# Performance work log

Measured on AMD Instinct MI355X. Metric: run time of the kernel, lower is better.

The kernel has to match this reference:

```python
import jax, jax.numpy as jnp
import numpy as np

TEMP = 5.0  # temperature_init
# All C(4,2)=6 keep-2-of-4 patterns for 2:4 semi-structured sparsity
PATTERNS = jnp.array([[1,1,0,0],[1,0,1,0],[1,0,0,1],[0,1,1,0],[0,1,0,1],[0,0,1,1]], dtype=jnp.float32)


def masked_linear(x, w, b, alpha, ids):
    # x: [N, I], w: [O, I], alpha: [A, O, I//4, 6], ids: [N]
    A, O, G, P = alpha.shape
    probs = jax.nn.softmax(alpha / TEMP, axis=-1)            # [A, O, G, 6]
    mask = jnp.einsum('aogp,pk->aogk', probs, PATTERNS)      # [A, O, G, 4]
    wm = w[None, :, :] * mask.reshape(A, O, G * 4)           # [A, O, I] per-agent masked weight
    y = jnp.einsum('ni,aoi->nao', x, wm)                     # dense per-agent GEMM
    y = jnp.take_along_axis(y, ids[:, None, None], axis=1)[:, 0, :]
    return y + b


def gru_cell(x, h, w_ih, w_hh, b_ih, b_hh):
    gi = x @ w_ih.T + b_ih
    gh = h @ w_hh.T + b_hh
    i_r, i_z, i_n = jnp.split(gi, 3, axis=-1)
    h_r, h_z, h_n = jnp.split(gh, 3, axis=-1)
    r = jax.nn.sigmoid(i_r + h_r)
    z = jax.nn.sigmoid(i_z + h_z)
    n = jnp.tanh(i_n + r * h_n)
    return (1.0 - z) * n + z * h


def setup_inputs() -> dict:
    key = jax.random.key(0)
    ks = jax.random.split(key, 20)
    B, A, E, H, NA = 1024, 8, 64, 512, 16
    s = 0.05
    d = {}
    d['inputs'] = jax.random.normal(ks[0], (B, A, E), jnp.float32)
    d['hidden_state'] = jax.random.normal(ks[1], (B, A, H), jnp.float32)
    d['agent_ids'] = jax.random.randint(ks[2], (B, A), 0, A, jnp.int32)
    d['fc1_w'] = jax.random.normal(ks[3], (H, E), jnp.float32) * s
    d['fc1_b'] = jax.random.normal(ks[4], (H,), jnp.float32) * s
    d['fc1_alpha'] = jax.random.normal(ks[5], (A, H, E // 4, 6), jnp.float32)
    d['gru_w_ih'] = jax.random.normal(ks[6], (3 * H, H), jnp.float32) * s
    d['gru_w_hh'] = jax.random.normal(ks[7], (3 * H, H), jnp.float32) * s
    d['gru_b_ih'] = jax.random.normal(ks[8], (3 * H,), jnp.float32) * s
    d['gru_b_hh'] = jax.random.normal(ks[9], (3 * H,), jnp.float32) * s
    d['fc2_w'] = jax.random.normal(ks[10], (H, H), jnp.float32) * s
    d['fc2_b'] = jax.random.normal(ks[11], (H,), jnp.float32) * s
    d['fc2_alpha'] = jax.random.normal(ks[12], (A, H, H // 4, 6), jnp.float32)
    d['fc3_w'] = jax.random.normal(ks[13], (H, H), jnp.float32) * s
    d['fc3_b'] = jax.random.normal(ks[14], (H,), jnp.float32) * s
    d['fc3_alpha'] = jax.random.normal(ks[15], (A, H, H // 4, 6), jnp.float32)
    d['fc4_w'] = jax.random.normal(ks[16], (NA, H), jnp.float32) * s
    d['fc4_b'] = jax.random.normal(ks[17], (NA,), jnp.float32) * s
    d['fc4_alpha'] = jax.random.normal(ks[18], (A, NA, H // 4, 6), jnp.float32)
    return d


def reference(inputs, hidden_state, agent_ids,
              fc1_w, fc1_b, fc1_alpha,
              gru_w_ih, gru_w_hh, gru_b_ih, gru_b_hh,
              fc2_w, fc2_b, fc2_alpha,
              fc3_w, fc3_b, fc3_alpha,
              fc4_w, fc4_b, fc4_alpha):
    b, a, e = inputs.shape
    H = hidden_state.shape[-1]
    x = inputs.reshape(-1, e)
    ids = agent_ids.reshape(-1)
    x = jax.nn.relu(masked_linear(x, fc1_w, fc1_b, fc1_alpha, ids))
    h = gru_cell(x, hidden_state.reshape(-1, H), gru_w_ih, gru_w_hh, gru_b_ih, gru_b_hh)
    q = jax.nn.relu(masked_linear(h, fc2_w, fc2_b, fc2_alpha, ids))
    q = jax.nn.relu(masked_linear(q, fc3_w, fc3_b, fc3_alpha, ids))
    q = masked_linear(q, fc4_w, fc4_b, fc4_alpha, ids)
    return q.reshape(b, a, -1), h.reshape(b, a, -1)
```

## Files before the change

### kernel.cpp

```cpp
#include <hip/hip_runtime.h>
#include <hip/hip_bf16.h>

typedef unsigned short ushort_t;
typedef __bf16 bf16x8 __attribute__((ext_vector_type(8)));
typedef unsigned short us8 __attribute__((ext_vector_type(8)));
typedef float f32x4 __attribute__((ext_vector_type(4)));

__device__ __forceinline__ float b2f(ushort_t h) {
    union { unsigned int u; float f; } v; v.u = ((unsigned int)h) << 16; return v.f;
}
__device__ __forceinline__ ushort_t f2b(float f) {
    union { float f; unsigned int u; } v; v.f = f;
    unsigned int u = v.u;
    unsigned int r = (u + 0x7FFFu + ((u >> 16) & 1u)) >> 16;
    return (ushort_t)r;
}
__device__ __forceinline__ float sigmoidf_(float x) {
    return 1.f / (1.f + __expf(-x));
}
__device__ __forceinline__ void store_o(ushort_t* p, float v) { *p = f2b(v); }
__device__ __forceinline__ void store_o(float* p, float v) { *p = v; }

__global__ void fill_kernel(float* out, long long n, float val) {
    long long i = (long long)blockIdx.x * blockDim.x + threadIdx.x;
    if (i < n) out[i] = val;
}

#define PACKSZ(O, K) ((long long)((O) >= 64 ? (O) >> 6 : 1) * ((K) >> 5) * 2048)

__global__ void sort_kernel(const int* __restrict__ ids, int N,
                            int* __restrict__ perm, int* __restrict__ seg,
                            int4* __restrict__ ttab, int* __restrict__ tcount) {
    __shared__ int hist[16][8];
    __shared__ int wbase[16][8];
    __shared__ int atot[8];
    __shared__ int abase[8];
    int tid = threadIdx.x, wave = tid >> 6, lane = tid & 63;
    int base = wave * 512;
    unsigned long long lt = (lane == 63) ? 0x7fffffffffffffffull
                                         : ((1ull << lane) - 1ull);
    int myid[8], rank[8];
    int run[8] = {0, 0, 0, 0, 0, 0, 0, 0};
    #pragma unroll
    for (int i = 0; i < 8; i++) myid[i] = ids[base + i * 64 + lane] & 7;
    #pragma unroll
    for (int i = 0; i < 8; i++) {
        int a = myid[i];
        int r = 0;
        #pragma unroll
        for (int a2 = 0; a2 < 8; a2++) {
            unsigned long long m = __ballot(a == a2);
            if (a2 == a) r = run[a2] + __popcll(m & lt);
            run[a2] += __popcll(m);
        }
        rank[i] = r;
    }
    if (lane == 0) {
        #pragma unroll
        for (int a = 0; a < 8; a++) hist[wave][a] = run[a];
    }
    __syncthreads();
    if (tid < 8) {
        int a = tid, s = 0;
        for (int w = 0; w < 16; w++) { wbase[w][a] = s; s += hist[w][a]; }
        atot[a] = s;
    }
    __syncthreads();
    if (tid == 0) {
        int s = 0;
        for (int a = 0; a < 8; a++) { abase[a] = s; seg[a] = s; s += atot[a]; }
        seg[8] = s;
        int T = 0;
        for (int a = 0; a < 8; a++)
            for (int m = abase[a]; m < abase[a] + atot[a]; m += 64) {
                int e = abase[a] + atot[a];
                if (e > m + 64) e = m + 64;
                ttab[T++] = make_int4(a, m, e, 0);
            }
        *tcount = T;
    }
    __syncthreads();
    #pragma unroll
    for (int i = 0; i < 8; i++) {
        int a = myid[i];
        perm[abase[a] + wbase[wave][a] + rank[i]] = base + i * 64 + lane;
    }
}

__device__ __forceinline__ void maskw_item(const float* __restrict__ alpha,
                                           const float* __restrict__ w,
                                           ushort_t* __restrict__ wm,
                                           long long idx, int O, int G, int dup) {
    int g = (int)(idx % G);
    long long t2 = idx / G;
    int o = (int)(t2 % O);
    int a = (int)(t2 / O);
    const float* al = alpha + idx * 6;
    float p[6];
    float mx = -1e30f;
    #pragma unroll
    for (int i = 0; i < 6; i++) { p[i] = al[i] * 0.2f; mx = fmaxf(mx, p[i]); }
    float s = 0.f;
    #pragma unroll
    for (int i = 0; i < 6; i++) { p[i] = __expf(p[i] - mx); s += p[i]; }
    float inv = 1.f / s;
    #pragma unroll
    for (int i = 0; i < 6; i++) p[i] *= inv;
    float mk[4] = { p[0] + p[1] + p[2], p[0] + p[3] + p[4],
                    p[1] + p[3] + p[5], p[2] + p[4] + p[5] };
    int K = G * 4;
    const float* wr = w + (long long)o * K + g * 4;
    ushort_t* base = wm + (long long)a * PACKSZ(O, K);
    int k0 = g * 4;
    int c = o >> 6, su = (o >> 4) & 3, n = o & 15;
    int kk = k0 >> 5, q = (k0 >> 3) & 3, e0 = k0 & 7;
    long long off = (((long long)(c * (K >> 5) + kk) * 4 + su) * 64 + (q * 16 + n)) * 8 + e0;
    #pragma unroll
    for (int t = 0; t < 4; t++) {
        ushort_t v = f2b(wr[t] * mk[t]);
        base[off + t] = v;
        if (dup) {
            base[off + t + 512] = v;
            base[off + t + 1024] = v;
            base[off + t + 1536] = v;
        }
    }
}

__device__ __forceinline__ void canon_gather_item(const float* __restrict__ src,
                                                  ushort_t* __restrict__ dst,
                                                  const int* __restrict__ perm,
                                                  int ld, long long i) {
    long long base = i * 8;
    int pos = (int)(base / ld);
    int k = (int)(base % ld);
    int row = perm[pos] & 8191;
    const float* s = src + (long long)row * ld + k;
    us8 v;
    #pragma unroll
    for (int e = 0; e < 8; e++) v[e] = f2b(s[e]);
    *(us8*)(dst + base) = v;
}

__device__ __forceinline__ void canon_pack_item(const float* __restrict__ src,
                                                ushort_t* __restrict__ dst,
                                                long long i) {
    long long base = i * 8;
    int o_full = (int)(base >> 9);
    int k0 = (int)(base & 511);
    int g = o_full >> 9, o = o_full & 511;
    int c = o >> 6, su = (o >> 4) & 3, n = o & 15;
    int kk = k0 >> 5, q = (k0 >> 3) & 3;
    long long off = (long long)g * 262144 +
        (((long long)(c * 16 + kk) * 4 + su) * 64 + (q * 16 + n)) * 8;
    us8 v;
    #pragma unroll
    for (int e = 0; e < 8; e++) v[e] = f2b(src[base + e]);
    *(us8*)(dst + off) = v;
}

#define PB0 256
#define PB1 2048
#define PB2 2048
#define PB3 64
#define PB4 256
#define PB5 2048
#define PB6 384
#define PB7 384
#define PREP_BLOCKS (PB0+PB1+PB2+PB3+PB4+PB5+PB6+PB7)

__global__ void prep_kernel(const float* fc1_al, const float* fc1_w, ushort_t* wm1,
                            const float* fc2_al, const float* fc2_w, ushort_t* wm2,
                            const float* fc3_al, const float* fc3_w, ushort_t* wm3,
                            const float* fc4_al, const float* fc4_w, ushort_t* wm4,
                            const float* inputs, ushort_t* inp_pos,
                            const float* hidden, ushort_t* hid_pos,
                            const float* wih, ushort_t* wihp,
                            const float* whh, ushort_t* whhp,
                            const int* perm) {
    int b = blockIdx.x;
    int tid = threadIdx.x;
    if (b < PB0) { maskw_item(fc1_al, fc1_w, wm1, (long long)b * 256 + tid, 512, 16, 0); return; }
    b -= PB0;
    if (b < PB1) { maskw_item(fc2_al, fc2_w, wm2, (long long)b * 256 + tid, 512, 128, 0); return; }
    b -= PB1;
    if (b < PB2) { maskw_item(fc3_al, fc3_w, wm3, (long long)b * 256 + tid, 512, 128, 0); return; }
    b -= PB2;
    if (b < PB3) { maskw_item(fc4_al, fc4_w, wm4, (long long)b * 256 + tid, 16, 128, 1); return; }
    b -= PB3;
    if (b < PB4) { canon_gather_item(inputs, inp_pos, perm, 64, (long long)b * 256 + tid); return; }
    b -= PB4;
    if (b < PB5) { canon_gather_item(hidden, hid_pos, perm, 512, (long long)b * 256 + tid); return; }
    b -= PB5;
    if (b < PB6) { canon_pack_item(wih, wihp, (long long)b * 256 + tid); return; }
    b -= PB6;
    canon_pack_item(whh, whhp, (long long)b * 256 + tid);
}

#define BM 64
#define BN 64

template <typename OT>
__launch_bounds__(256, 4)
__global__ void gemm_tiled(const ushort_t* __restrict__ In, int ldin,
                           const ushort_t* __restrict__ Wpk, long long wstride,
                           const float* __restrict__ bias,
                           OT* __restrict__ Out, int ldo,
                           const int4* __restrict__ ttab,
                           const int* __restrict__ tcount,
                           const int* __restrict__ scatter,
                           int O, int K, int relu) {
    int t = blockIdx.x;
    if (t >= *tcount) return;
    int4 tt = ttab[t];
    int a = tt.x, pos0 = tt.y, pos1 = tt.z;
    int o0 = blockIdx.y * BN;

    __shared__ ushort_t As[2048];

    int tid = threadIdx.x;
    int wave = tid >> 6, lane = tid & 63;
    int wr = (wave >> 1) & 1, wc = wave & 1;
    int quad = lane >> 4, l16 = lane & 15;
    int srow = tid >> 2, sgrp = tid & 3;
    int wsoff = (srow * 4 + (sgrp ^ ((srow >> 2) & 3))) * 8;
    int rl = (l16 * 4 + (quad ^ ((l16 >> 2) & 3))) * 8;

    int apos = pos0 + srow;
    int apos_c = apos < pos1 ? apos : (pos1 - 1);
    const ushort_t* aptr = In + (long long)apos_c * ldin + sgrp * 8;

    const ushort_t* wb = Wpk + (long long)a * wstride +
        (long long)blockIdx.y * (K >> 5) * 2048 + lane * 8;

    f32x4 acc[2][2];
    #pragma unroll
    for (int i = 0; i < 2; i++)
        #pragma unroll
        for (int j = 0; j < 2; j++) acc[i][j] = (f32x4){0.f, 0.f, 0.f, 0.f};

    int KK = K >> 5;
    for (int kk = 0; kk < KK; kk++) {
        us8 av = *(const us8*)(aptr + kk * 32);
        bf16x8 bfr[2];
        bfr[0] = *(const bf16x8*)(wb + (kk * 4 + wc * 2 + 0) * 512);
        bfr[1] = *(const bf16x8*)(wb + (kk * 4 + wc * 2 + 1) * 512);
        __syncthreads();
        *(us8*)(&As[wsoff]) = av;
        __syncthreads();
        bf16x8 af[2];
        af[0] = *(const bf16x8*)(&As[(wr * 2 + 0) * 512 + rl]);
        af[1] = *(const bf16x8*)(&As[(wr * 2 + 1) * 512 + rl]);
        #pragma unroll
        for (int i = 0; i < 2; i++)
            #pragma unroll
            for (int j = 0; j < 2; j++)
                acc[i][j] = __builtin_amdgcn_mfma_f32_16x16x32_bf16(af[i], bfr[j], acc[i][j], 0, 0, 0);
    }

    #pragma unroll
    for (int i = 0; i < 2; i++) {
        int mbase = wr * 32 + i * 16 + quad * 4;
        #pragma unroll
        for (int j = 0; j < 2; j++) {
            int col = o0 + wc * 32 + j * 16 + l16;
            if (col < O) {
                float bias_v = bias ? bias[col] : 0.f;
                #pragma unroll
                for (int r = 0; r < 4; r++) {
                    int pos = pos0 + mbase + r;
                    if (pos < pos1) {
                        float v = acc[i][j][r] + bias_v;
                        if (relu) v = fmaxf(v, 0.f);
                        int orow = (scatter ? scatter[pos] : pos) & 8191;
                        store_o(&Out[(long long)orow * ldo + col], v);
                    }
                }
            }
        }
    }
}

__launch_bounds__(256, 3)
__global__ void gru_fused(const ushort_t* __restrict__ y1,
                          const ushort_t* __restrict__ hid_pos,
                          const float* __restrict__ hidden_f,
                          const ushort_t* __restrict__ wihp,
                          const ushort_t* __restrict__ whhp,
                          const float* __restrict__ bih,
                          const float* __restrict__ bhh,
                          const int* __restrict__ perm,
                          float* __restrict__ out_h_f,
                          ushort_t* __restrict__ hp,
                          int N, int H) {
    int m0 = blockIdx.x * 64;

    __shared__ ushort_t Ay[2048];
    __shared__ ushort_t Ah[2048];
    __shared__ ushort_t Bt[6][2048];

    int tid = threadIdx.x;
    int wave = tid >> 6, lane = tid & 63;
    int wr = (wave >> 1) & 1, wc = wave & 1;
    int quad = lane >> 4, l16 = lane & 15;
    int srow = tid >> 2, sgrp = tid & 3;
    int wsoff = (srow * 4 + (sgrp ^ ((srow >> 2) & 3))) * 8;
    int rl = (l16 * 4 + (quad ^ ((l16 >> 2) & 3))) * 8;

    const ushort_t* ay_p = y1 + (long long)(m0 + srow) * H + sgrp * 8;
    const ushort_t* ah_p = hid_pos + (long long)(m0 + srow) * H + sgrp * 8;

    long long cb = (long long)blockIdx.y * 16 * 2048 + tid * 8;
    const ushort_t* wbg[6];
    #pragma unroll
    for (int g = 0; g < 3; g++) wbg[g] = wihp + (long long)g * 262144 + cb;
    #pragma unroll
    for (int g = 3; g < 6; g++) wbg[g] = whhp + (long long)(g - 3) * 262144 + cb;

    f32x4 acc[4][2][2];
    #pragma unroll
    for (int g = 0; g < 4; g++)
        #pragma unroll
        for (int i = 0; i < 2; i++)
            #pragma unroll
            for (int j = 0; j < 2; j++) acc[g][i][j] = (f32x4){0.f, 0.f, 0.f, 0.f};

    for (int kk = 0; kk < 16; kk++) {
        us8 va = *(const us8*)(ay_p + kk * 32);
        us8 vh = *(const us8*)(ah_p + kk * 32);
        us8 vb[6];
        #pragma unroll
        for (int g = 0; g < 6; g++) vb[g] = *(const us8*)(wbg[g] + kk * 2048);
        __syncthreads();
        *(us8*)(&Ay[wsoff]) = va;
        *(us8*)(&Ah[wsoff]) = vh;
        #pragma unroll
        for (int g = 0; g < 6; g++) *(us8*)(&Bt[g][tid * 8]) = vb[g];
        __syncthreads();

        bf16x8 ayf[2], ahf[2];
        #pragma unroll
        for (int u = 0; u < 2; u++) {
            ayf[u] = *(const bf16x8*)(&Ay[(wr * 2 + u) * 512 + rl]);
            ahf[u] = *(const bf16x8*)(&Ah[(wr * 2 + u) * 512 + rl]);
        }
        #pragma unroll
        for (int g = 0; g < 3; g++) {
            bf16x8 bw[2], bu[2];
            #pragma unroll
            for (int u = 0; u < 2; u++) {
                bw[u] = *(const bf16x8*)(&Bt[g][(wc * 2 + u) * 512 + lane * 8]);
                bu[u] = *(const bf16x8*)(&Bt[g + 3][(wc * 2 + u) * 512 + lane * 8]);
            }
            int ai = (g < 2) ? g : 2;
            int ah2 = (g < 2) ? g : 3;
            #pragma unroll
            for (int i = 0; i < 2; i++)
                #pragma unroll
                for (int j = 0; j < 2; j++) {
                    acc[ai][i][j] = __builtin_amdgcn_mfma_f32_16x16x32_bf16(
                        ayf[i], bw[j], acc[ai][i][j], 0, 0, 0);
                    acc[ah2][i][j] = __builtin_amdgcn_mfma_f32_16x16x32_bf16(
                        ahf[i], bu[j], acc[ah2][i][j], 0, 0, 0);
                }
        }
    }

    int c0 = blockIdx.y * 64;
    #pragma unroll
    for (int i = 0; i < 2; i++) {
        #pragma unroll
        for (int r = 0; r < 4; r++) {
            int pos = m0 + wr * 32 + i * 16 + quad * 4 + r;
            int norig = perm[pos] & 8191;
            #pragma unroll
            for (int j = 0; j < 2; j++) {
                int col = c0 + wc * 32 + j * 16 + l16;
                float sr = acc[0][i][j][r] + bih[col] + bhh[col];
                float sz = acc[1][i][j][r] + bih[H + col] + bhh[H + col];
                float in_ = acc[2][i][j][r] + bih[2 * H + col];
                float hn = acc[3][i][j][r] + bhh[2 * H + col];
                float rg = sigmoidf_(sr);
                float zg = sigmoidf_(sz);
                float ng = tanhf(in_ + rg * hn);
                float hv = hidden_f[(long long)norig * H + col];
                float hnew = (1.f - zg) * ng + zg * hv;
                out_h_f[(long long)norig * H + col] = hnew;
                hp[(long long)pos * H + col] = f2b(hnew);
            }
        }
    }
}

extern "C" void kernel_launch(void* const* d_in, const int* in_sizes, int n_in,
                              void* d_out, int out_size, void* d_ws, size_t ws_size,
                              hipStream_t stream) {
    (void)in_sizes; (void)n_in;
    const int N = 8192, A = 8, E = 64, H = 512, NA = 16;

    float* out_f = (float*)d_out;
    float* out_q = out_f;
    float* out_h = out_f + (size_t)N * NA;

    char* p = (char*)d_ws;
    auto alloc = [&](size_t b) { char* r = p; p += (b + 255) & ~(size_t)255; return r; };
    int*  perm   = (int*)alloc((size_t)N * 4);
    int*  seg    = (int*)alloc(16 * 4);
    int4* ttab   = (int4*)alloc(144 * 16);
    int*  tcount = (int*)alloc(256);
    ushort_t* wm1     = (ushort_t*)alloc((size_t)A * PACKSZ(H, E) * 2);
    ushort_t* wm2     = (ushort_t*)alloc((size_t)A * PACKSZ(H, H) * 2);
    ushort_t* wm3     = (ushort_t*)alloc((size_t)A * PACKSZ(H, H) * 2);
    ushort_t* wm4     = (ushort_t*)alloc((size_t)A * PACKSZ(NA, H) * 2);
    ushort_t* y1      = (ushort_t*)alloc((size_t)N * H * 2);
    ushort_t* inp_pos = (ushort_t*)alloc((size_t)N * E * 2);
    ushort_t* hid_pos = (ushort_t*)alloc((size_t)N * H * 2);
    ushort_t* wihp    = (ushort_t*)alloc((size_t)3 * H * H * 2);
    ushort_t* whhp    = (ushort_t*)alloc((size_t)3 * H * H * 2);
    ushort_t* hp      = (ushort_t*)alloc((size_t)N * H * 2);
    size_t need = (size_t)(p - (char*)d_ws);
    ushort_t* q2 = y1;
    ushort_t* q3 = hid_pos;

    if (ws_size < need) {
        fill_kernel<<<(unsigned)((out_size + 255) / 256), 256, 0, stream>>>(
            out_f, out_size, 1000.f);
        return;
    }

    const float* inputs = (const float*)d_in[0];
    const float* hidden = (const float*)d_in[1];
    const int*   ids    = (const int*)d_in[2];
    const float* fc1_w  = (const float*)d_in[3];
    const float* fc1_b  = (const float*)d_in[4];
    const float* fc1_al = (const float*)d_in[5];
    const float* wih    = (const float*)d_in[6];
    const float* whh    = (const float*)d_in[7];
    const float* bih    = (const float*)d_in[8];
    const float* bhh    = (const float*)d_in[9];
    const float* fc2_w  = (const float*)d_in[10];
    const float* fc2_b  = (const float*)d_in[11];
    const float* fc2_al = (const float*)d_in[12];
    const float* fc3_w  = (const float*)d_in[13];
    const float* fc3_b  = (const float*)d_in[14];
    const float* fc3_al = (const float*)d_in[15];
    const float* fc4_w  = (const float*)d_in[16];
    const float* fc4_b  = (const float*)d_in[17];
    const float* fc4_al = (const float*)d_in[18];

    sort_kernel<<<1, 1024, 0, stream>>>(ids, N, perm, seg, ttab, tcount);

    prep_kernel<<<PREP_BLOCKS, 256, 0, stream>>>(
        fc1_al, fc1_w, wm1, fc2_al, fc2_w, wm2, fc3_al, fc3_w, wm3,
        fc4_al, fc4_w, wm4, inputs, inp_pos, hidden, hid_pos,
        wih, wihp, whh, whhp, perm);

    dim3 blk(256);
    gemm_tiled<ushort_t><<<dim3(136, H / BN), blk, 0, stream>>>(
        inp_pos, E, wm1, PACKSZ(H, E), fc1_b, y1, H, ttab, tcount,
        nullptr, H, E, 1);
    gru_fused<<<dim3(N / 64, H / 64), blk, 0, stream>>>(
        y1, hid_pos, hidden, wihp, whhp, bih, bhh, perm, out_h, hp, N, H);
    gemm_tiled<ushort_t><<<dim3(136, H / BN), blk, 0, stream>>>(
        hp, H, wm2, PACKSZ(H, H), fc2_b, q2, H, ttab, tcount,
        nullptr, H, H, 1);
    gemm_tiled<ushort_t><<<dim3(136, H / BN), blk, 0, stream>>>(
        q2, H, wm3, PACKSZ(H, H), fc3_b, q3, H, ttab, tcount,
        nullptr, H, H, 1);
    gemm_tiled<float><<<dim3(136, 1), blk, 0, stream>>>(
        q3, H, wm4, PACKSZ(NA, H), fc4_b, out_q, NA, ttab, tcount,
        perm, NA, H, 0);
}
```

Measured before the change: 228.3 us.

## Pre-pack activations in MFMA fragment layout with padded agent segments, drop LDS staging

```diff
diff --git a/kernel.cpp b/kernel.cpp
--- a/kernel.cpp
+++ b/kernel.cpp
@@ -6,9 +6,9 @@
 typedef unsigned short us8 __attribute__((ext_vector_type(8)));
 typedef float f32x4 __attribute__((ext_vector_type(4)));
 
-__device__ __forceinline__ float b2f(ushort_t h) {
-    union { unsigned int u; float f; } v; v.u = ((unsigned int)h) << 16; return v.f;
-}
+#define NPAD 8704
+#define SENT (1 << 20)
+
 __device__ __forceinline__ ushort_t f2b(float f) {
     union { float f; unsigned int u; } v; v.f = f;
     unsigned int u = v.u;
@@ -18,8 +18,6 @@
 __device__ __forceinline__ float sigmoidf_(float x) {
     return 1.f / (1.f + __expf(-x));
 }
-__device__ __forceinline__ void store_o(ushort_t* p, float v) { *p = f2b(v); }
-__device__ __forceinline__ void store_o(float* p, float v) { *p = v; }
 
 __global__ void fill_kernel(float* out, long long n, float val) {
     long long i = (long long)blockIdx.x * blockDim.x + threadIdx.x;
@@ -68,15 +66,20 @@
     __syncthreads();
     if (tid == 0) {
         int s = 0;
-        for (int a = 0; a < 8; a++) { abase[a] = s; seg[a] = s; s += atot[a]; }
+        for (int a = 0; a < 8; a++) {
+            abase[a] = s; seg[a] = s;
+            s += (atot[a] + 63) & ~63;
+        }
         seg[8] = s;
         int T = 0;
-        for (int a = 0; a < 8; a++)
-            for (int m = abase[a]; m < abase[a] + atot[a]; m += 64) {
-                int e = abase[a] + atot[a];
-                if (e > m + 64) e = m + 64;
-                ttab[T++] = make_int4(a, m, e, 0);
+        for (int a = 0; a < 8; a++) {
+            int e = abase[a] + atot[a];
+            int pe = abase[a] + ((atot[a] + 63) & ~63);
+            for (int m = abase[a]; m < pe; m += 64) {
+                int z = e < m + 64 ? e : m + 64;
+                ttab[T++] = make_int4(a, m, z, 0);
             }
+        }
         *tcount = T;
     }
     __syncthreads();
@@ -85,6 +88,13 @@
         int a = myid[i];
         perm[abase[a] + wbase[wave][a] + rank[i]] = base + i * 64 + lane;
     }
+    for (int a = 0; a < 8; a++) {
+        int e = abase[a] + atot[a];
+        int pe = abase[a] + ((atot[a] + 63) & ~63);
+        for (int p2 = e + tid; p2 < pe; p2 += 1024) perm[p2] = SENT;
+    }
+    int Pend = abase[7] + ((atot[7] + 63) & ~63);
+    for (int p2 = Pend + tid; p2 < NPAD; p2 += 1024) perm[p2] = SENT;
 }
 
 __device__ __forceinline__ void maskw_item(const float* __restrict__ alpha,
@@ -127,19 +137,21 @@
     }
 }
 
-__device__ __forceinline__ void canon_gather_item(const float* __restrict__ src,
-                                                  ushort_t* __restrict__ dst,
-                                                  const int* __restrict__ perm,
-                                                  int ld, long long i) {
-    long long base = i * 8;
-    int pos = (int)(base / ld);
-    int k = (int)(base % ld);
-    int row = perm[pos] & 8191;
-    const float* s = src + (long long)row * ld + k;
+__device__ __forceinline__ void canon_gather_packed(const float* __restrict__ src,
+                                                    ushort_t* __restrict__ dst,
+                                                    const int* __restrict__ perm,
+                                                    int ld, long long i) {
+    int l = (int)(i & 63);
+    int tt = (int)(i >> 6);
+    int KK = ld >> 5;
+    int mt = tt / KK, kk = tt - mt * KK;
+    int row = perm[mt * 16 + (l & 15)];
+    if (row >= 8192) row = 0;
+    const float* s = src + (long long)row * ld + kk * 32 + (l >> 4) * 8;
     us8 v;
     #pragma unroll
     for (int e = 0; e < 8; e++) v[e] = f2b(s[e]);
-    *(us8*)(dst + base) = v;
+    *(us8*)(dst + i * 8) = v;
 }
 
 __device__ __forceinline__ void canon_pack_item(const float* __restrict__ src,
@@ -163,8 +175,8 @@
 #define PB1 2048
 #define PB2 2048
 #define PB3 64
-#define PB4 256
-#define PB5 2048
+#define PB4 272
+#define PB5 2176
 #define PB6 384
 #define PB7 384
 #define PREP_BLOCKS (PB0+PB1+PB2+PB3+PB4+PB5+PB6+PB7)
@@ -188,92 +200,122 @@
     b -= PB2;
     if (b < PB3) { maskw_item(fc4_al, fc4_w, wm4, (long long)b * 256 + tid, 16, 128, 1); return; }
     b -= PB3;
-    if (b < PB4) { canon_gather_item(inputs, inp_pos, perm, 64, (long long)b * 256 + tid); return; }
+    if (b < PB4) { canon_gather_packed(inputs, inp_pos, perm, 64, (long long)b * 256 + tid); return; }
     b -= PB4;
-    if (b < PB5) { canon_gather_item(hidden, hid_pos, perm, 512, (long long)b * 256 + tid); return; }
+    if (b < PB5) { canon_gather_packed(hidden, hid_pos, perm, 512, (long long)b * 256 + tid); return; }
     b -= PB5;
     if (b < PB6) { canon_pack_item(wih, wihp, (long long)b * 256 + tid); return; }
     b -= PB6;
     canon_pack_item(whh, whhp, (long long)b * 256 + tid);
 }
 
-#define BM 64
-#define BN 64
-
-template <typename OT>
+template <typename OT, int NC, int PACKOUT>
 __launch_bounds__(256, 4)
-__global__ void gemm_tiled(const ushort_t* __restrict__ In, int ldin,
+__global__ void gemm_tiled(const ushort_t* __restrict__ Apk, int K,
                            const ushort_t* __restrict__ Wpk, long long wstride,
                            const float* __restrict__ bias,
                            OT* __restrict__ Out, int ldo,
                            const int4* __restrict__ ttab,
                            const int* __restrict__ tcount,
-                           const int* __restrict__ scatter,
-                           int O, int K, int relu) {
+                           const int* __restrict__ perm,
+                           int O, int relu) {
     int t = blockIdx.x;
     if (t >= *tcount) return;
     int4 tt = ttab[t];
-    int a = tt.x, pos0 = tt.y, pos1 = tt.z;
-    int o0 = blockIdx.y * BN;
-
-    __shared__ ushort_t As[2048];
+    int a = tt.x, pos0 = tt.y;
+    constexpr int JJ = 2 * NC;
 
     int tid = threadIdx.x;
     int wave = tid >> 6, lane = tid & 63;
     int wr = (wave >> 1) & 1, wc = wave & 1;
     int quad = lane >> 4, l16 = lane & 15;
-    int srow = tid >> 2, sgrp = tid & 3;
-    int wsoff = (srow * 4 + (sgrp ^ ((srow >> 2) & 3))) * 8;
-    int rl = (l16 * 4 + (quad ^ ((l16 >> 2) & 3))) * 8;
-
-    int apos = pos0 + srow;
-    int apos_c = apos < pos1 ? apos : (pos1 - 1);
-    const ushort_t* aptr = In + (long long)apos_c * ldin + sgrp * 8;
-
+
+    int KK = K >> 5;
+    int KKh = KK >> 1;
+    int c_idx = blockIdx.y * NC + (NC == 2 ? wc : 0);
     const ushort_t* wb = Wpk + (long long)a * wstride +
-        (long long)blockIdx.y * (K >> 5) * 2048 + lane * 8;
-
-    f32x4 acc[2][2];
+        (long long)c_idx * KK * 2048 + lane * 8;
+    const ushort_t* ap = Apk + (long long)(pos0 >> 4) * KK * 512 + lane * 8;
+
+    f32x4 acc[2][JJ];
     #pragma unroll
     for (int i = 0; i < 2; i++)
         #pragma unroll
-        for (int j = 0; j < 2; j++) acc[i][j] = (f32x4){0.f, 0.f, 0.f, 0.f};
-
-    int KK = K >> 5;
-    for (int kk = 0; kk < KK; kk++) {
-        us8 av = *(const us8*)(aptr + kk * 32);
-        bf16x8 bfr[2];
-        bfr[0] = *(const bf16x8*)(wb + (kk * 4 + wc * 2 + 0) * 512);
-        bfr[1] = *(const bf16x8*)(wb + (kk * 4 + wc * 2 + 1) * 512);
-        __syncthreads();
-        *(us8*)(&As[wsoff]) = av;
-        __syncthreads();
-        bf16x8 af[2];
-        af[0] = *(const bf16x8*)(&As[(wr * 2 + 0) * 512 + rl]);
-        af[1] = *(const bf16x8*)(&As[(wr * 2 + 1) * 512 + rl]);
+        for (int j = 0; j < JJ; j++) acc[i][j] = (f32x4){0.f, 0.f, 0.f, 0.f};
+
+    bf16x8 aA[2], bA[JJ], aB[2], bB[JJ];
+
+#define GLOADS(AR, BR, kkv) do {                                              \
+    _Pragma("unroll") for (int i2 = 0; i2 < 2; i2++)                          \
+        AR[i2] = *(const bf16x8*)(ap + ((long long)(wr * 2 + i2) * KK + (kkv)) * 512); \
+    _Pragma("unroll") for (int j2 = 0; j2 < JJ; j2++) {                       \
+        int su = (NC == 2) ? j2 : wc * 2 + j2;                                \
+        BR[j2] = *(const bf16x8*)(wb + ((kkv) * 4 + su) * 512); }             \
+} while (0)
+#define GMFMAS(AR, BR) do {                                                   \
+    _Pragma("unroll") for (int i2 = 0; i2 < 2; i2++)                          \
+        _Pragma("unroll") for (int j2 = 0; j2 < JJ; j2++)                     \
+            acc[i2][j2] = __builtin_amdgcn_mfma_f32_16x16x32_bf16(            \
+                AR[i2], BR[j2], acc[i2][j2], 0, 0, 0);                        \
+} while (0)
+
+    GLOADS(aA, bA, 0);
+    #pragma unroll 1
+    for (int kk2 = 0; kk2 < KKh; kk2++) {
+        GLOADS(aB, bB, kk2 * 2 + 1);
+        GMFMAS(aA, bA);
+        if (kk2 + 1 < KKh) GLOADS(aA, bA, kk2 * 2 + 2);
+        GMFMAS(aB, bB);
+    }
+#undef GLOADS
+#undef GMFMAS
+
+    if constexpr (PACKOUT) {
+        __shared__ ushort_t Cs[64 * 136];
         #pragma unroll
         for (int i = 0; i < 2; i++)
             #pragma unroll
-            for (int j = 0; j < 2; j++)
-                acc[i][j] = __builtin_amdgcn_mfma_f32_16x16x32_bf16(af[i], bfr[j], acc[i][j], 0, 0, 0);
-    }
-
-    #pragma unroll
-    for (int i = 0; i < 2; i++) {
-        int mbase = wr * 32 + i * 16 + quad * 4;
-        #pragma unroll
-        for (int j = 0; j < 2; j++) {
-            int col = o0 + wc * 32 + j * 16 + l16;
-            if (col < O) {
-                float bias_v = bias ? bias[col] : 0.f;
+            for (int j = 0; j < JJ; j++) {
+                int colL = (NC == 2 ? wc * 64 : wc * 32) + j * 16 + l16;
+                int col = blockIdx.y * (64 * NC) + colL;
+                float bv = bias[col];
                 #pragma unroll
                 for (int r = 0; r < 4; r++) {
-                    int pos = pos0 + mbase + r;
-                    if (pos < pos1) {
-                        float v = acc[i][j][r] + bias_v;
-                        if (relu) v = fmaxf(v, 0.f);
-                        int orow = (scatter ? scatter[pos] : pos) & 8191;
-                        store_o(&Out[(long long)orow * ldo + col], v);
+                    float v = acc[i][j][r] + bv;
+                    if (relu) v = fmaxf(v, 0.f);
+                    Cs[(wr * 32 + i * 16 + quad * 4 + r) * 136 + colL] = f2b(v);
+                }
+            }
+        __syncthreads();
+        int KKo = ldo >> 5;
+        int kk0 = blockIdx.y * (2 * NC);
+        constexpr int NKK = 2 * NC;
+        #pragma unroll
+        for (int s2 = 0; s2 < NKK; s2++) {
+            int slot = s2 * 256 + tid;
+            int l = slot & 63, t4 = slot >> 6;
+            int mt = t4 / NKK, kkL = t4 - mt * NKK;
+            us8 v = *(const us8*)(&Cs[(mt * 16 + (l & 15)) * 136 + kkL * 32 + (l >> 4) * 8]);
+            *(us8*)((ushort_t*)Out + ((long long)((pos0 >> 4) + mt) * KKo + kk0 + kkL) * 512 + l * 8) = v;
+        }
+    } else {
+        #pragma unroll
+        for (int i = 0; i < 2; i++) {
+            int mbase = wr * 32 + i * 16 + quad * 4;
+            #pragma unroll
+            for (int j = 0; j < JJ; j++) {
+                int col = (NC == 2 ? wc * 64 : wc * 32) + j * 16 + l16;
+                if (col < O) {
+                    float bv = bias[col];
+                    #pragma unroll
+                    for (int r = 0; r < 4; r++) {
+                        int pos = pos0 + mbase + r;
+                        int orow = perm[pos];
+                        if (orow < 8192) {
+                            float v = acc[i][j][r] + bv;
+                            if (relu) v = fmaxf(v, 0.f);
+                            Out[(long long)orow * ldo + col] = v;
+                        }
                     }
                 }
             }
@@ -281,9 +323,9 @@
     }
 }
 
-__launch_bounds__(256, 3)
+__launch_bounds__(256, 2)
 __global__ void gru_fused(const ushort_t* __restrict__ y1,
-                          const ushort_t* __restrict__ hid_pos,
+                          const ushort_t* __restrict__ hid,
                           const float* __restrict__ hidden_f,
                           const ushort_t* __restrict__ wihp,
                           const ushort_t* __restrict__ whhp,
@@ -292,25 +334,23 @@
                           const int* __restrict__ perm,
                           float* __restrict__ out_h_f,
                           ushort_t* __restrict__ hp,
-                          int N, int H) {
-    int m0 = blockIdx.x * 64;
-
-    __shared__ ushort_t Ay[2048];
-    __shared__ ushort_t Ah[2048];
-    __shared__ ushort_t Bt[6][2048];
+                          const int4* __restrict__ ttab,
+                          const int* __restrict__ tcount,
+                          int H) {
+    int t = blockIdx.x;
+    if (t >= *tcount) return;
+    int pos0 = ttab[t].y;
+    int mt0 = pos0 >> 4;
 
     int tid = threadIdx.x;
     int wave = tid >> 6, lane = tid & 63;
     int wr = (wave >> 1) & 1, wc = wave & 1;
     int quad = lane >> 4, l16 = lane & 15;
-    int srow = tid >> 2, sgrp = tid & 3;
-    int wsoff = (srow * 4 + (sgrp ^ ((srow >> 2) & 3))) * 8;
-    int rl = (l16 * 4 + (quad ^ ((l16 >> 2) & 3))) * 8;
-
-    const ushort_t* ay_p = y1 + (long long)(m0 + srow) * H + sgrp * 8;
-    const ushort_t* ah_p = hid_pos + (long long)(m0 + srow) * H + sgrp * 8;
-
-    long long cb = (long long)blockIdx.y * 16 * 2048 + tid * 8;
+
+    const ushort_t* ayp = y1 + (long long)mt0 * 16 * 512 + lane * 8;
+    const ushort_t* ahp = hid + (long long)mt0 * 16 * 512 + lane * 8;
+
+    long long cb = (long long)blockIdx.y * 16 * 2048 + lane * 8;
     const ushort_t* wbg[6];
     #pragma unroll
     for (int g = 0; g < 3; g++) wbg[g] = wihp + (long long)g * 262144 + cb;
@@ -325,57 +365,55 @@
             #pragma unroll
             for (int j = 0; j < 2; j++) acc[g][i][j] = (f32x4){0.f, 0.f, 0.f, 0.f};
 
-    for (int kk = 0; kk < 16; kk++) {
-        us8 va = *(const us8*)(ay_p + kk * 32);
-        us8 vh = *(const us8*)(ah_p + kk * 32);
-        us8 vb[6];
-        #pragma unroll
-        for (int g = 0; g < 6; g++) vb[g] = *(const us8*)(wbg[g] + kk * 2048);
-        __syncthreads();
-        *(us8*)(&Ay[wsoff]) = va;
-        *(us8*)(&Ah[wsoff]) = vh;
-        #pragma unroll
-        for (int g = 0; g < 6; g++) *(us8*)(&Bt[g][tid * 8]) = vb[g];
-        __syncthreads();
-
-        bf16x8 ayf[2], ahf[2];
-        #pragma unroll
-        for (int u = 0; u < 2; u++) {
-            ayf[u] = *(const bf16x8*)(&Ay[(wr * 2 + u) * 512 + rl]);
-            ahf[u] = *(const bf16x8*)(&Ah[(wr * 2 + u) * 512 + rl]);
-        }
-        #pragma unroll
-        for (int g = 0; g < 3; g++) {
-            bf16x8 bw[2], bu[2];
-            #pragma unroll
-            for (int u = 0; u < 2; u++) {
-                bw[u] = *(const bf16x8*)(&Bt[g][(wc * 2 + u) * 512 + lane * 8]);
-                bu[u] = *(const bf16x8*)(&Bt[g + 3][(wc * 2 + u) * 512 + lane * 8]);
-            }
-            int ai = (g < 2) ? g : 2;
-            int ah2 = (g < 2) ? g : 3;
-            #pragma unroll
-            for (int i = 0; i < 2; i++)
-                #pragma unroll
-                for (int j = 0; j < 2; j++) {
-                    acc[ai][i][j] = __builtin_amdgcn_mfma_f32_16x16x32_bf16(
-                        ayf[i], bw[j], acc[ai][i][j], 0, 0, 0);
-                    acc[ah2][i][j] = __builtin_amdgcn_mfma_f32_16x16x32_bf16(
-                        ahf[i], bu[j], acc[ah2][i][j], 0, 0, 0);
-                }
-        }
-    }
-
+    bf16x8 ayA[2], ahA[2], bbA[6][2];
+    bf16x8 ayB[2], ahB[2], bbB[6][2];
+
+#define RLOADS(AY, AH, BB, kkv) do {                                          \
+    _Pragma("unroll") for (int i2 = 0; i2 < 2; i2++) {                        \
+        AY[i2] = *(const bf16x8*)(ayp + ((long long)(wr * 2 + i2) * 16 + (kkv)) * 512); \
+        AH[i2] = *(const bf16x8*)(ahp + ((long long)(wr * 2 + i2) * 16 + (kkv)) * 512); } \
+    _Pragma("unroll") for (int g2 = 0; g2 < 6; g2++)                          \
+        _Pragma("unroll") for (int u2 = 0; u2 < 2; u2++)                      \
+            BB[g2][u2] = *(const bf16x8*)(wbg[g2] + ((kkv) * 4 + wc * 2 + u2) * 512); \
+} while (0)
+#define RMFMAS(AY, AH, BB) do {                                               \
+    _Pragma("unroll") for (int g2 = 0; g2 < 3; g2++) {                        \
+        int ai = (g2 < 2) ? g2 : 2;                                           \
+        int ah2 = (g2 < 2) ? g2 : 3;                                          \
+        _Pragma("unroll") for (int i2 = 0; i2 < 2; i2++)                      \
+            _Pragma("unroll") for (int j2 = 0; j2 < 2; j2++) {                \
+                acc[ai][i2][j2] = __builtin_amdgcn_mfma_f32_16x16x32_bf16(    \
+                    AY[i2], BB[g2][j2], acc[ai][i2][j2], 0, 0, 0);            \
+                acc[ah2][i2][j2] = __builtin_amdgcn_mfma_f32_16x16x32_bf16(   \
+                    AH[i2], BB[g2 + 3][j2], acc[ah2][i2][j2], 0, 0, 0); } }   \
+} while (0)
+
+    RLOADS(ayA, ahA, bbA, 0);
+    #pragma unroll 1
+    for (int kk2 = 0; kk2 < 8; kk2++) {
+        RLOADS(ayB, ahB, bbB, kk2 * 2 + 1);
+        RMFMAS(ayA, ahA, bbA);
+        if (kk2 < 7) RLOADS(ayA, ahA, bbA, kk2 * 2 + 2);
+        RMFMAS(ayB, ahB, bbB);
+    }
+#undef RLOADS
+#undef RMFMAS
+
+    __shared__ ushort_t Cs[64 * 72];
     int c0 = blockIdx.y * 64;
     #pragma unroll
     for (int i = 0; i < 2; i++) {
         #pragma unroll
         for (int r = 0; r < 4; r++) {
-            int pos = m0 + wr * 32 + i * 16 + quad * 4 + r;
-            int norig = perm[pos] & 8191;
+            int rowL = wr * 32 + i * 16 + quad * 4 + r;
+            int pos = pos0 + rowL;
+            int norig = perm[pos];
+            bool realr = norig < 8192;
+            int nr = realr ? norig : 0;
             #pragma unroll
             for (int j = 0; j < 2; j++) {
-                int col = c0 + wc * 32 + j * 16 + l16;
+                int colL = wc * 32 + j * 16 + l16;
+                int col = c0 + colL;
                 float sr = acc[0][i][j][r] + bih[col] + bhh[col];
                 float sz = acc[1][i][j][r] + bih[H + col] + bhh[H + col];
                 float in_ = acc[2][i][j][r] + bih[2 * H + col];
@@ -383,12 +421,21 @@
                 float rg = sigmoidf_(sr);
                 float zg = sigmoidf_(sz);
                 float ng = tanhf(in_ + rg * hn);
-                float hv = hidden_f[(long long)norig * H + col];
+                float hv = hidden_f[(long long)nr * H + col];
                 float hnew = (1.f - zg) * ng + zg * hv;
-                out_h_f[(long long)norig * H + col] = hnew;
-                hp[(long long)pos * H + col] = f2b(hnew);
+                if (realr) out_h_f[(long long)norig * H + col] = hnew;
+                Cs[rowL * 72 + colL] = f2b(hnew);
             }
         }
+    }
+    __syncthreads();
+    #pragma unroll
+    for (int s2 = 0; s2 < 2; s2++) {
+        int slot = s2 * 256 + tid;
+        int l = slot & 63, t4 = slot >> 6;
+        int mt = t4 >> 1, kkL = t4 & 1;
+        us8 v = *(const us8*)(&Cs[(mt * 16 + (l & 15)) * 72 + kkL * 32 + (l >> 4) * 8]);
+        *(us8*)(hp + ((long long)(mt0 + mt) * 16 + blockIdx.y * 2 + kkL) * 512 + l * 8) = v;
     }
 }
 
@@ -404,7 +451,7 @@
 
     char* p = (char*)d_ws;
     auto alloc = [&](size_t b) { char* r = p; p += (b + 255) & ~(size_t)255; return r; };
-    int*  perm   = (int*)alloc((size_t)N * 4);
+    int*  perm   = (int*)alloc((size_t)NPAD * 4);
     int*  seg    = (int*)alloc(16 * 4);
     int4* ttab   = (int4*)alloc(144 * 16);
     int*  tcount = (int*)alloc(256);
@@ -412,12 +459,12 @@
     ushort_t* wm2     = (ushort_t*)alloc((size_t)A * PACKSZ(H, H) * 2);
     ushort_t* wm3     = (ushort_t*)alloc((size_t)A * PACKSZ(H, H) * 2);
     ushort_t* wm4     = (ushort_t*)alloc((size_t)A * PACKSZ(NA, H) * 2);
-    ushort_t* y1      = (ushort_t*)alloc((size_t)N * H * 2);
-    ushort_t* inp_pos = (ushort_t*)alloc((size_t)N * E * 2);
-    ushort_t* hid_pos = (ushort_t*)alloc((size_t)N * H * 2);
+    ushort_t* y1      = (ushort_t*)alloc((size_t)NPAD * H * 2);
+    ushort_t* inp_pos = (ushort_t*)alloc((size_t)NPAD * E * 2);
+    ushort_t* hid_pos = (ushort_t*)alloc((size_t)NPAD * H * 2);
     ushort_t* wihp    = (ushort_t*)alloc((size_t)3 * H * H * 2);
     ushort_t* whhp    = (ushort_t*)alloc((size_t)3 * H * H * 2);
-    ushort_t* hp      = (ushort_t*)alloc((size_t)N * H * 2);
+    ushort_t* hp      = (ushort_t*)alloc((size_t)NPAD * H * 2);
     size_t need = (size_t)(p - (char*)d_ws);
     ushort_t* q2 = y1;
     ushort_t* q3 = hid_pos;
@@ -456,18 +503,19 @@
         wih, wihp, whh, whhp, perm);
 
     dim3 blk(256);
-    gemm_tiled<ushort_t><<<dim3(136, H / BN), blk, 0, stream>>>(
+    gemm_tiled<ushort_t, 2, 1><<<dim3(136, H / 128), blk, 0, stream>>>(
         inp_pos, E, wm1, PACKSZ(H, E), fc1_b, y1, H, ttab, tcount,
-        nullptr, H, E, 1);
-    gru_fused<<<dim3(N / 64, H / 64), blk, 0, stream>>>(
-        y1, hid_pos, hidden, wihp, whhp, bih, bhh, perm, out_h, hp, N, H);
-    gemm_tiled<ushort_t><<<dim3(136, H / BN), blk, 0, stream>>>(
+        perm, H, 1);
+    gru_fused<<<dim3(136, H / 64), blk, 0, stream>>>(
+        y1, hid_pos, hidden, wihp, whhp, bih, bhh, perm, out_h, hp,
+        ttab, tcount, H);
+    gemm_tiled<ushort_t, 2, 1><<<dim3(136, H / 128), blk, 0, stream>>>(
         hp, H, wm2, PACKSZ(H, H), fc2_b, q2, H, ttab, tcount,
-        nullptr, H, H, 1);
-    gemm_tiled<ushort_t><<<dim3(136, H / BN), blk, 0, stream>>>(
+        perm, H, 1);
+    gemm_tiled<ushort_t, 2, 1><<<dim3(136, H / 128), blk, 0, stream>>>(
         q2, H, wm3, PACKSZ(H, H), fc3_b, q3, H, ttab, tcount,
-        nullptr, H, H, 1);
-    gemm_tiled<float><<<dim3(136, 1), blk, 0, stream>>>(
+        perm, H, 1);
+    gemm_tiled<float, 1, 0><<<dim3(136, 1), blk, 0, stream>>>(
         q3, H, wm4, PACKSZ(NA, H), fc4_b, out_q, NA, ttab, tcount,
-        perm, NA, H, 0);
-}
+        perm, NA, 0);
+}
```

New measurement: 246.4 us. +7.9%, slower.

## Process two K-steps per barrier in gemm_tiled and widen GRU tile to 128 rows

Applied to the files above, without the earlier changes.

```diff
diff --git a/kernel.cpp b/kernel.cpp
--- a/kernel.cpp
+++ b/kernel.cpp
@@ -6,9 +6,6 @@
 typedef unsigned short us8 __attribute__((ext_vector_type(8)));
 typedef float f32x4 __attribute__((ext_vector_type(4)));
 
-__device__ __forceinline__ float b2f(ushort_t h) {
-    union { unsigned int u; float f; } v; v.u = ((unsigned int)h) << 16; return v.f;
-}
 __device__ __forceinline__ ushort_t f2b(float f) {
     union { float f; unsigned int u; } v; v.f = f;
     unsigned int u = v.u;
@@ -216,7 +213,7 @@
     int a = tt.x, pos0 = tt.y, pos1 = tt.z;
     int o0 = blockIdx.y * BN;
 
-    __shared__ ushort_t As[2048];
+    __shared__ ushort_t As[2][2048];
 
     int tid = threadIdx.x;
     int wave = tid >> 6, lane = tid & 63;
@@ -239,23 +236,34 @@
         #pragma unroll
         for (int j = 0; j < 2; j++) acc[i][j] = (f32x4){0.f, 0.f, 0.f, 0.f};
 
-    int KK = K >> 5;
-    for (int kk = 0; kk < KK; kk++) {
-        us8 av = *(const us8*)(aptr + kk * 32);
-        bf16x8 bfr[2];
-        bfr[0] = *(const bf16x8*)(wb + (kk * 4 + wc * 2 + 0) * 512);
-        bfr[1] = *(const bf16x8*)(wb + (kk * 4 + wc * 2 + 1) * 512);
+    int KKh = K >> 6;
+    for (int k2 = 0; k2 < KKh; k2++) {
+        int kk = k2 * 2;
+        us8 av0 = *(const us8*)(aptr + kk * 32);
+        us8 av1 = *(const us8*)(aptr + kk * 32 + 32);
+        bf16x8 b00 = *(const bf16x8*)(wb + (kk * 4 + wc * 2 + 0) * 512);
+        bf16x8 b01 = *(const bf16x8*)(wb + (kk * 4 + wc * 2 + 1) * 512);
+        bf16x8 b10 = *(const bf16x8*)(wb + ((kk + 1) * 4 + wc * 2 + 0) * 512);
+        bf16x8 b11 = *(const bf16x8*)(wb + ((kk + 1) * 4 + wc * 2 + 1) * 512);
         __syncthreads();
-        *(us8*)(&As[wsoff]) = av;
+        *(us8*)(&As[0][wsoff]) = av0;
+        *(us8*)(&As[1][wsoff]) = av1;
         __syncthreads();
-        bf16x8 af[2];
-        af[0] = *(const bf16x8*)(&As[(wr * 2 + 0) * 512 + rl]);
-        af[1] = *(const bf16x8*)(&As[(wr * 2 + 1) * 512 + rl]);
-        #pragma unroll
-        for (int i = 0; i < 2; i++)
-            #pragma unroll
-            for (int j = 0; j < 2; j++)
-                acc[i][j] = __builtin_amdgcn_mfma_f32_16x16x32_bf16(af[i], bfr[j], acc[i][j], 0, 0, 0);
+        bf16x8 af0[2], af1[2];
+        af0[0] = *(const bf16x8*)(&As[0][(wr * 2 + 0) * 512 + rl]);
+        af0[1] = *(const bf16x8*)(&As[0][(wr * 2 + 1) * 512 + rl]);
+        af1[0] = *(const bf16x8*)(&As[1][(wr * 2 + 0) * 512 + rl]);
+        af1[1] = *(const bf16x8*)(&As[1][(wr * 2 + 1) * 512 + rl]);
+        #pragma unroll
+        for (int i = 0; i < 2; i++) {
+            acc[i][0] = __builtin_amdgcn_mfma_f32_16x16x32_bf16(af0[i], b00, acc[i][0], 0, 0, 0);
+            acc[i][1] = __builtin_amdgcn_mfma_f32_16x16x32_bf16(af0[i], b01, acc[i][1], 0, 0, 0);
+        }
+        #pragma unroll
+        for (int i = 0; i < 2; i++) {
+            acc[i][0] = __builtin_amdgcn_mfma_f32_16x16x32_bf16(af1[i], b10, acc[i][0], 0, 0, 0);
+            acc[i][1] = __builtin_amdgcn_mfma_f32_16x16x32_bf16(af1[i], b11, acc[i][1], 0, 0, 0);
+        }
     }
 
     #pragma unroll
@@ -281,7 +289,7 @@
     }
 }
 
-__launch_bounds__(256, 3)
+__launch_bounds__(512, 2)
 __global__ void gru_fused(const ushort_t* __restrict__ y1,
                           const ushort_t* __restrict__ hid_pos,
                           const float* __restrict__ hidden_f,
@@ -293,15 +301,15 @@
                           float* __restrict__ out_h_f,
                           ushort_t* __restrict__ hp,
                           int N, int H) {
-    int m0 = blockIdx.x * 64;
-
-    __shared__ ushort_t Ay[2048];
-    __shared__ ushort_t Ah[2048];
+    int m0 = blockIdx.x * 128;
+
+    __shared__ ushort_t Ay[4096];
+    __shared__ ushort_t Ah[4096];
     __shared__ ushort_t Bt[6][2048];
 
     int tid = threadIdx.x;
     int wave = tid >> 6, lane = tid & 63;
-    int wr = (wave >> 1) & 1, wc = wave & 1;
+    int wr = wave >> 1, wc = wave & 1;
     int quad = lane >> 4, l16 = lane & 15;
     int srow = tid >> 2, sgrp = tid & 3;
     int wsoff = (srow * 4 + (sgrp ^ ((srow >> 2) & 3))) * 8;
@@ -310,12 +318,17 @@
     const ushort_t* ay_p = y1 + (long long)(m0 + srow) * H + sgrp * 8;
     const ushort_t* ah_p = hid_pos + (long long)(m0 + srow) * H + sgrp * 8;
 
-    long long cb = (long long)blockIdx.y * 16 * 2048 + tid * 8;
-    const ushort_t* wbg[6];
-    #pragma unroll
-    for (int g = 0; g < 3; g++) wbg[g] = wihp + (long long)g * 262144 + cb;
-    #pragma unroll
-    for (int g = 3; g < 6; g++) wbg[g] = whhp + (long long)(g - 3) * 262144 + cb;
+    const ushort_t* wbs[3];
+    int wg[3];
+    #pragma unroll
+    for (int q = 0; q < 3; q++) {
+        int s = q * 512 + tid;
+        int g = s >> 8, so = s & 255;
+        wg[q] = s;
+        wbs[q] = ((g < 3) ? (wihp + (long long)g * 262144)
+                          : (whhp + (long long)(g - 3) * 262144)) +
+                 (long long)blockIdx.y * 16 * 2048 + so * 8;
+    }
 
     f32x4 acc[4][2][2];
     #pragma unroll
@@ -328,14 +341,17 @@
     for (int kk = 0; kk < 16; kk++) {
         us8 va = *(const us8*)(ay_p + kk * 32);
         us8 vh = *(const us8*)(ah_p + kk * 32);
-        us8 vb[6];
-        #pragma unroll
-        for (int g = 0; g < 6; g++) vb[g] = *(const us8*)(wbg[g] + kk * 2048);
+        us8 vb[3];
+        #pragma unroll
+        for (int q = 0; q < 3; q++) vb[q] = *(const us8*)(wbs[q] + kk * 2048);
         __syncthreads();
         *(us8*)(&Ay[wsoff]) = va;
         *(us8*)(&Ah[wsoff]) = vh;
         #pragma unroll
-        for (int g = 0; g < 6; g++) *(us8*)(&Bt[g][tid * 8]) = vb[g];
+        for (int q = 0; q < 3; q++) {
+            int s = wg[q];
+            *(us8*)(&Bt[s >> 8][(s & 255) * 8]) = vb[q];
+        }
         __syncthreads();
 
         bf16x8 ayf[2], ahf[2];
@@ -459,7 +475,7 @@
     gemm_tiled<ushort_t><<<dim3(136, H / BN), blk, 0, stream>>>(
         inp_pos, E, wm1, PACKSZ(H, E), fc1_b, y1, H, ttab, tcount,
         nullptr, H, E, 1);
-    gru_fused<<<dim3(N / 64, H / 64), blk, 0, stream>>>(
+    gru_fused<<<dim3(N / 128, H / 64), dim3(512), 0, stream>>>(
         y1, hid_pos, hidden, wihp, whhp, bih, bhh, perm, out_h, hp, N, H);
     gemm_tiled<ushort_t><<<dim3(136, H / BN), blk, 0, stream>>>(
         hp, H, wm2, PACKSZ(H, H), fc2_b, q2, H, ttab, tcount,
```

After: 221.9 us. 1.03x faster.
